# Kernel optimization log

Measured on AMD Instinct MI355X. Metric: run time of the kernel, lower is better.

Reference implementation:

```python
import jax, jax.numpy as jnp
import numpy as np

F = 1024
K = 32
N = 2048
EPS = 1e-6


def setup_inputs() -> dict:
    key = jax.random.key(0)
    ks = jax.random.split(key, 10)
    x = jax.random.normal(ks[0], (N, F), dtype=jnp.float32)
    idx = jax.random.randint(ks[1], (F, K), 0, F)
    norm_w = jnp.ones((F,), dtype=jnp.float32)
    w1 = jax.random.normal(ks[2], (F, K), dtype=jnp.float32) / np.sqrt(K)
    b1 = jnp.zeros((F,), dtype=jnp.float32)
    w2 = jax.random.normal(ks[3], (F, K), dtype=jnp.float32) / np.sqrt(K)
    b2 = jnp.zeros((F,), dtype=jnp.float32)
    amp = jnp.ones((F,), dtype=jnp.float32)
    freq = jnp.ones((F,), dtype=jnp.float32)
    decay = jnp.full((F,), 0.01, dtype=jnp.float32)
    alpha = jnp.ones((1,), dtype=jnp.float32)
    return {"x": x, "in_index_per_out": idx, "norm_w": norm_w,
            "w1": w1, "b1": b1, "amp": amp, "freq": freq, "decay": decay,
            "w2": w2, "b2": b2, "alpha": alpha}


def _rmsnorm(x, g):
    ms = jnp.mean(x * x, axis=-1, keepdims=True)
    return x * jax.lax.rsqrt(ms + EPS) * g


def _geo_sparse_linear(h, idx, w, b):
    hg = h[:, idx]
    return jnp.einsum('nok,ok->no', hg, w) + b


def _sine_param(z, amp, freq, decay):
    return amp * jnp.sin(freq * z) * jnp.exp(-decay * z * z)


def reference(x, in_index_per_out, norm_w, w1, b1, amp, freq, decay, w2, b2, alpha):
    h = _rmsnorm(x, norm_w)
    h = _sine_param(_geo_sparse_linear(h, in_index_per_out, w1, b1), amp, freq, decay)
    h = _geo_sparse_linear(h, in_index_per_out, w2, b2)
    return x + alpha * h
```

## Files before the change

### kernel.cpp

```cpp
#include <hip/hip_runtime.h>
#include <hip/hip_fp16.h>

#define FDIM 1024
#define KNZ 32
#define NROWS 2048
#define RB 8
#define TPB 1024
#define EPSV 1e-6f

static_assert(TPB == FDIM, "o = tid mapping requires TPB == FDIM");
static_assert(NROWS % RB == 0, "rows divide");

__device__ __forceinline__ unsigned int swz(unsigned int i) {
  return i ^ ((i >> 3) & 7u);
}

__device__ __forceinline__ unsigned f16bits(float f) {
  return (unsigned)__half_as_ushort(__float2half(f));
}

__global__ void geo_prep(const int* __restrict__ idx,
                         const float* __restrict__ w1,
                         const float* __restrict__ w2,
                         unsigned* __restrict__ pr1, unsigned* __restrict__ pr2) {
  const int tid = threadIdx.x;
  const int lane = tid & 63;
  const int grp = (lane >> 5);
  const int k = tid & 31;
  const int o = blockIdx.x * 8 + (tid >> 5);

  const unsigned off = swz((unsigned)idx[o * KNZ + k]);
  const int q = (int)(off & 7u);
  const int ob = o & 7;
  const int qr = (q - ob) & 7;

  const unsigned long long gmask = 0xFFFFFFFFull << (32 * grp);
  const unsigned long long lowmask = (1ull << lane) - 1ull;

  unsigned long long m[8];
  #pragma unroll
  for (int qq = 0; qq < 8; ++qq) m[qq] = __ballot(q == qq) & gmask;

  unsigned long long mym = 0;
  #pragma unroll
  for (int qq = 0; qq < 8; ++qq) mym = (q == qq) ? m[qq] : mym;
  const int r = __popcll(mym & lowmask);

  int pos = 0;
  #pragma unroll
  for (int qq = 0; qq < 8; ++qq) {
    const int c = (int)__popcll(m[qq]);
    const int qqr = (qq - ob) & 7;
    pos += (r < c) ? r : c;
    pos += (qqr < qr && c > r) ? 1 : 0;
  }

  const unsigned e1 = (f16bits(w1[o * KNZ + k]) << 16) | off;
  const unsigned e2 = (f16bits(w2[o * KNZ + k]) << 16) | off;
  pr1[pos * FDIM + o] = e1;
  pr2[pos * FDIM + o] = e2;
}

__device__ __forceinline__ void gatherh(unsigned e, const uint4* lds,
                                        __half2* acc2) {
  unsigned wd = (e & 0xFFFF0000u) | (e >> 16);
  __half2 w = *reinterpret_cast<__half2*>(&wd);
  uint4 hv = lds[e & 1023u];
  const unsigned* hd = reinterpret_cast<const unsigned*>(&hv);
  #pragma unroll
  for (int d = 0; d < 4; ++d) {
    __half2 h2 = *reinterpret_cast<const __half2*>(&hd[d]);
    acc2[d] = __hfma2(h2, w, acc2[d]);
  }
}

template <bool TR>
__global__ __launch_bounds__(TPB, 4)
void geo_main(const float* __restrict__ x, const float* __restrict__ norm_w,
              const float* __restrict__ b1, const float* __restrict__ amp,
              const float* __restrict__ freq, const float* __restrict__ decay,
              const float* __restrict__ b2, const float* __restrict__ alpha,
              const unsigned* __restrict__ pr1, const unsigned* __restrict__ pr2,
              const int* __restrict__ idx, const float* __restrict__ w1,
              const float* __restrict__ w2, float* __restrict__ out) {
  __shared__ uint4 h_lds[FDIM];
  __shared__ uint4 s_lds[FDIM];
  __shared__ float red[(TPB / 64) * RB];
  __shared__ float rs_sh[RB];

  const int tid = threadIdx.x;
  const int lane = tid & 63;
  const int wid = tid >> 6;
  const int r0 = blockIdx.x * RB;
  const int o = tid;

  {
    float v[RB];
    #pragma unroll
    for (int r = 0; r < RB; ++r)
      v[r] = x[(r0 + r) * FDIM + tid];

    const float g = norm_w[tid];

    float p[RB];
    #pragma unroll
    for (int r = 0; r < RB; ++r) p[r] = v[r] * v[r];
    #pragma unroll
    for (int r = 0; r < 4; ++r) {
      float up = __shfl_xor(p[r + 4], 4, 64);
      float dn = __shfl_xor(p[r], 4, 64);
      p[r] = (lane & 4) ? (p[r + 4] + up) : (p[r] + dn);
    }
    #pragma unroll
    for (int r = 0; r < 2; ++r) {
      float up = __shfl_xor(p[r + 2], 2, 64);
      float dn = __shfl_xor(p[r], 2, 64);
      p[r] = (lane & 2) ? (p[r + 2] + up) : (p[r] + dn);
    }
    {
      float up = __shfl_xor(p[1], 1, 64);
      float dn = __shfl_xor(p[0], 1, 64);
      p[0] = (lane & 1) ? (p[1] + up) : (p[0] + dn);
    }
    p[0] += __shfl_xor(p[0], 8, 64);
    p[0] += __shfl_xor(p[0], 16, 64);
    p[0] += __shfl_xor(p[0], 32, 64);
    if (lane < RB) red[wid * RB + lane] = p[0];

    uint4 h;
    __half2 h01 = __floats2half2_rn(g * v[0], g * v[1]);
    __half2 h23 = __floats2half2_rn(g * v[2], g * v[3]);
    __half2 h45 = __floats2half2_rn(g * v[4], g * v[5]);
    __half2 h67 = __floats2half2_rn(g * v[6], g * v[7]);
    h.x = *reinterpret_cast<unsigned*>(&h01);
    h.y = *reinterpret_cast<unsigned*>(&h23);
    h.z = *reinterpret_cast<unsigned*>(&h45);
    h.w = *reinterpret_cast<unsigned*>(&h67);
    h_lds[swz((unsigned)tid)] = h;
  }

  __syncthreads();

  {
    float a = red[lane] + red[64 + lane];
    a += __shfl_xor(a, 8, 64);
    a += __shfl_xor(a, 16, 64);
    a += __shfl_xor(a, 32, 64);
    if (lane < RB) rs_sh[lane] = rsqrtf(a * (1.0f / FDIM) + EPSV);
  }

  __half2 acc2[4];
  {
    unsigned z = 0;
    #pragma unroll
    for (int d = 0; d < 4; ++d) acc2[d] = *reinterpret_cast<__half2*>(&z);
  }

  if (TR) {
    #pragma unroll
    for (int gk = 0; gk < 4; ++gk) {
      unsigned u[8];
      #pragma unroll
      for (int j = 0; j < 8; ++j) u[j] = pr1[(gk * 8 + j) * FDIM + o];
      #pragma unroll
      for (int j = 0; j < 8; ++j) gatherh(u[j], h_lds, acc2);
    }
  } else {
    #pragma unroll 8
    for (int k = 0; k < KNZ; ++k) {
      unsigned off = swz((unsigned)idx[o * KNZ + k]);
      unsigned e = (f16bits(w1[o * KNZ + k]) << 16) | off;
      gatherh(e, h_lds, acc2);
    }
  }

  {
    const float bb1 = b1[o], am = amp[o], fq = freq[o], dc = decay[o];
    const float4 ra = *reinterpret_cast<const float4*>(&rs_sh[0]);
    const float4 rb = *reinterpret_cast<const float4*>(&rs_sh[4]);
    const float rsv[RB] = {ra.x, ra.y, ra.z, ra.w, rb.x, rb.y, rb.z, rb.w};
    float accf[RB];
    #pragma unroll
    for (int d = 0; d < 4; ++d) {
      float2 f = __half22float2(acc2[d]);
      accf[2 * d] = f.x; accf[2 * d + 1] = f.y;
    }
    float s[RB];
    #pragma unroll
    for (int r = 0; r < RB; ++r) {
      float z = fmaf(accf[r], rsv[r], bb1);
      s[r] = am * __sinf(fq * z) * __expf(-dc * z * z);
    }
    uint4 sv;
    __half2 s01 = __floats2half2_rn(s[0], s[1]);
    __half2 s23 = __floats2half2_rn(s[2], s[3]);
    __half2 s45 = __floats2half2_rn(s[4], s[5]);
    __half2 s67 = __floats2half2_rn(s[6], s[7]);
    sv.x = *reinterpret_cast<unsigned*>(&s01);
    sv.y = *reinterpret_cast<unsigned*>(&s23);
    sv.z = *reinterpret_cast<unsigned*>(&s45);
    sv.w = *reinterpret_cast<unsigned*>(&s67);
    s_lds[swz((unsigned)o)] = sv;
  }
  __syncthreads();

  {
    unsigned z = 0;
    #pragma unroll
    for (int d = 0; d < 4; ++d) acc2[d] = *reinterpret_cast<__half2*>(&z);
  }

  if (TR) {
    #pragma unroll
    for (int gk = 0; gk < 4; ++gk) {
      unsigned u[8];
      #pragma unroll
      for (int j = 0; j < 8; ++j) u[j] = pr2[(gk * 8 + j) * FDIM + o];
      #pragma unroll
      for (int j = 0; j < 8; ++j) gatherh(u[j], s_lds, acc2);
    }
  } else {
    #pragma unroll 8
    for (int k = 0; k < KNZ; ++k) {
      unsigned off = swz((unsigned)idx[o * KNZ + k]);
      unsigned e = (f16bits(w2[o * KNZ + k]) << 16) | off;
      gatherh(e, s_lds, acc2);
    }
  }

  {
    const float bb2 = b2[o];
    const float al = alpha[0];
    float accf[RB];
    #pragma unroll
    for (int d = 0; d < 4; ++d) {
      float2 f = __half22float2(acc2[d]);
      accf[2 * d] = f.x; accf[2 * d + 1] = f.y;
    }
    #pragma unroll
    for (int r = 0; r < RB; ++r)
      out[(r0 + r) * FDIM + o] =
          fmaf(al, accf[r] + bb2, x[(r0 + r) * FDIM + o]);
  }
}

extern "C" void kernel_launch(void* const* d_in, const int* in_sizes, int n_in,
                              void* d_out, int out_size, void* d_ws, size_t ws_size,
                              hipStream_t stream) {
  const float* x      = (const float*)d_in[0];
  const int*   idx    = (const int*)d_in[1];
  const float* norm_w = (const float*)d_in[2];
  const float* w1     = (const float*)d_in[3];
  const float* b1     = (const float*)d_in[4];
  const float* amp    = (const float*)d_in[5];
  const float* freq   = (const float*)d_in[6];
  const float* decay  = (const float*)d_in[7];
  const float* w2     = (const float*)d_in[8];
  const float* b2     = (const float*)d_in[9];
  const float* alpha  = (const float*)d_in[10];
  float* out = (float*)d_out;

  const size_t need = 2ull * FDIM * KNZ * sizeof(unsigned);
  if (ws_size >= need) {
    unsigned* pr1 = (unsigned*)d_ws;
    unsigned* pr2 = pr1 + (size_t)FDIM * KNZ;
    geo_prep<<<FDIM / 8, 256, 0, stream>>>(idx, w1, w2, pr1, pr2);
    geo_main<true><<<NROWS / RB, TPB, 0, stream>>>(
        x, norm_w, b1, amp, freq, decay, b2, alpha, pr1, pr2, idx, w1, w2, out);
  } else {
    geo_main<false><<<NROWS / RB, TPB, 0, stream>>>(
        x, norm_w, b1, amp, freq, decay, b2, alpha, nullptr, nullptr, idx, w1, w2, out);
  }
}
```

Before: 19.84 us.

## Halve rows per block to 4 and redo LDS bank-conflict sort for 8-byte entries

Rows per block drop from 8 to 4, so each LDS entry becomes a uint2 of four fp16 values instead of a uint4 of eight. The XOR swizzle is removed, and the prep kernel now sorts gather entries into 16 bank groups instead of 8 to spread conflicts for the smaller element size. The launch-bounds occupancy hint rises from 4 to 8 blocks and the grid doubles. The goal is more resident blocks and cheaper LDS traffic, at the cost of loading the index and weight stream twice as often per row.

```diff
diff --git a/kernel.cpp b/kernel.cpp
--- a/kernel.cpp
+++ b/kernel.cpp
@@ -4,19 +4,20 @@
 #define FDIM 1024
 #define KNZ 32
 #define NROWS 2048
-#define RB 8
+#define RB 4
 #define TPB 1024
 #define EPSV 1e-6f
 
 static_assert(TPB == FDIM, "o = tid mapping requires TPB == FDIM");
 static_assert(NROWS % RB == 0, "rows divide");
 
-__device__ __forceinline__ unsigned int swz(unsigned int i) {
-  return i ^ ((i >> 3) & 7u);
-}
-
 __device__ __forceinline__ unsigned f16bits(float f) {
   return (unsigned)__half_as_ushort(__float2half(f));
+}
+
+__device__ __forceinline__ unsigned packh2(float a, float b) {
+  __half2 h = __floats2half2_rn(a, b);
+  return *reinterpret_cast<unsigned*>(&h);
 }
 
 __global__ void geo_prep(const int* __restrict__ idx,
@@ -29,53 +30,49 @@
   const int k = tid & 31;
   const int o = blockIdx.x * 8 + (tid >> 5);
 
-  const unsigned off = swz((unsigned)idx[o * KNZ + k]);
-  const int q = (int)(off & 7u);
-  const int ob = o & 7;
-  const int qr = (q - ob) & 7;
+  const unsigned off = (unsigned)idx[o * KNZ + k] & 1023u;
+  const int q = (int)(off & 15u);
+  const int ob = o & 15;
+  const int qr = (q - ob) & 15;
 
   const unsigned long long gmask = 0xFFFFFFFFull << (32 * grp);
   const unsigned long long lowmask = (1ull << lane) - 1ull;
 
-  unsigned long long m[8];
+  unsigned long long m[16];
   #pragma unroll
-  for (int qq = 0; qq < 8; ++qq) m[qq] = __ballot(q == qq) & gmask;
+  for (int qq = 0; qq < 16; ++qq) m[qq] = __ballot(q == qq) & gmask;
 
   unsigned long long mym = 0;
   #pragma unroll
-  for (int qq = 0; qq < 8; ++qq) mym = (q == qq) ? m[qq] : mym;
+  for (int qq = 0; qq < 16; ++qq) mym = (q == qq) ? m[qq] : mym;
   const int r = __popcll(mym & lowmask);
 
   int pos = 0;
   #pragma unroll
-  for (int qq = 0; qq < 8; ++qq) {
+  for (int qq = 0; qq < 16; ++qq) {
     const int c = (int)__popcll(m[qq]);
-    const int qqr = (qq - ob) & 7;
+    const int qqr = (qq - ob) & 15;
     pos += (r < c) ? r : c;
     pos += (qqr < qr && c > r) ? 1 : 0;
   }
 
-  const unsigned e1 = (f16bits(w1[o * KNZ + k]) << 16) | off;
-  const unsigned e2 = (f16bits(w2[o * KNZ + k]) << 16) | off;
-  pr1[pos * FDIM + o] = e1;
-  pr2[pos * FDIM + o] = e2;
-}
-
-__device__ __forceinline__ void gatherh(unsigned e, const uint4* lds,
+  pr1[pos * FDIM + o] = (f16bits(w1[o * KNZ + k]) << 16) | off;
+  pr2[pos * FDIM + o] = (f16bits(w2[o * KNZ + k]) << 16) | off;
+}
+
+__device__ __forceinline__ void gatherh(unsigned e, const uint2* lds,
                                         __half2* acc2) {
   unsigned wd = (e & 0xFFFF0000u) | (e >> 16);
   __half2 w = *reinterpret_cast<__half2*>(&wd);
-  uint4 hv = lds[e & 1023u];
-  const unsigned* hd = reinterpret_cast<const unsigned*>(&hv);
-  #pragma unroll
-  for (int d = 0; d < 4; ++d) {
-    __half2 h2 = *reinterpret_cast<const __half2*>(&hd[d]);
-    acc2[d] = __hfma2(h2, w, acc2[d]);
-  }
+  uint2 hv = lds[e & 1023u];
+  __half2 h0 = *reinterpret_cast<const __half2*>(&hv.x);
+  __half2 h1 = *reinterpret_cast<const __half2*>(&hv.y);
+  acc2[0] = __hfma2(h0, w, acc2[0]);
+  acc2[1] = __hfma2(h1, w, acc2[1]);
 }
 
 template <bool TR>
-__global__ __launch_bounds__(TPB, 4)
+__global__ __launch_bounds__(TPB, 8)
 void geo_main(const float* __restrict__ x, const float* __restrict__ norm_w,
               const float* __restrict__ b1, const float* __restrict__ amp,
               const float* __restrict__ freq, const float* __restrict__ decay,
@@ -83,8 +80,8 @@
               const unsigned* __restrict__ pr1, const unsigned* __restrict__ pr2,
               const int* __restrict__ idx, const float* __restrict__ w1,
               const float* __restrict__ w2, float* __restrict__ out) {
-  __shared__ uint4 h_lds[FDIM];
-  __shared__ uint4 s_lds[FDIM];
+  __shared__ uint2 h_lds[FDIM];
+  __shared__ uint2 s_lds[FDIM];
   __shared__ float red[(TPB / 64) * RB];
   __shared__ float rs_sh[RB];
 
@@ -106,12 +103,6 @@
     #pragma unroll
     for (int r = 0; r < RB; ++r) p[r] = v[r] * v[r];
     #pragma unroll
-    for (int r = 0; r < 4; ++r) {
-      float up = __shfl_xor(p[r + 4], 4, 64);
-      float dn = __shfl_xor(p[r], 4, 64);
-      p[r] = (lane & 4) ? (p[r + 4] + up) : (p[r] + dn);
-    }
-    #pragma unroll
     for (int r = 0; r < 2; ++r) {
       float up = __shfl_xor(p[r + 2], 2, 64);
       float dn = __shfl_xor(p[r], 2, 64);
@@ -122,38 +113,34 @@
       float dn = __shfl_xor(p[0], 1, 64);
       p[0] = (lane & 1) ? (p[1] + up) : (p[0] + dn);
     }
+    p[0] += __shfl_xor(p[0], 4, 64);
     p[0] += __shfl_xor(p[0], 8, 64);
     p[0] += __shfl_xor(p[0], 16, 64);
     p[0] += __shfl_xor(p[0], 32, 64);
     if (lane < RB) red[wid * RB + lane] = p[0];
 
-    uint4 h;
-    __half2 h01 = __floats2half2_rn(g * v[0], g * v[1]);
-    __half2 h23 = __floats2half2_rn(g * v[2], g * v[3]);
-    __half2 h45 = __floats2half2_rn(g * v[4], g * v[5]);
-    __half2 h67 = __floats2half2_rn(g * v[6], g * v[7]);
-    h.x = *reinterpret_cast<unsigned*>(&h01);
-    h.y = *reinterpret_cast<unsigned*>(&h23);
-    h.z = *reinterpret_cast<unsigned*>(&h45);
-    h.w = *reinterpret_cast<unsigned*>(&h67);
-    h_lds[swz((unsigned)tid)] = h;
+    uint2 h;
+    h.x = packh2(g * v[0], g * v[1]);
+    h.y = packh2(g * v[2], g * v[3]);
+    h_lds[tid] = h;
   }
 
   __syncthreads();
 
   {
-    float a = red[lane] + red[64 + lane];
+    float a = red[lane];
+    a += __shfl_xor(a, 4, 64);
     a += __shfl_xor(a, 8, 64);
     a += __shfl_xor(a, 16, 64);
     a += __shfl_xor(a, 32, 64);
     if (lane < RB) rs_sh[lane] = rsqrtf(a * (1.0f / FDIM) + EPSV);
   }
 
-  __half2 acc2[4];
+  __half2 acc2[2];
   {
     unsigned z = 0;
-    #pragma unroll
-    for (int d = 0; d < 4; ++d) acc2[d] = *reinterpret_cast<__half2*>(&z);
+    acc2[0] = *reinterpret_cast<__half2*>(&z);
+    acc2[1] = *reinterpret_cast<__half2*>(&z);
   }
 
   if (TR) {
@@ -168,8 +155,8 @@
   } else {
     #pragma unroll 8
     for (int k = 0; k < KNZ; ++k) {
-      unsigned off = swz((unsigned)idx[o * KNZ + k]);
-      unsigned e = (f16bits(w1[o * KNZ + k]) << 16) | off;
+      unsigned e = (f16bits(w1[o * KNZ + k]) << 16) |
+                   ((unsigned)idx[o * KNZ + k] & 1023u);
       gatherh(e, h_lds, acc2);
     }
   }
@@ -177,13 +164,12 @@
   {
     const float bb1 = b1[o], am = amp[o], fq = freq[o], dc = decay[o];
     const float4 ra = *reinterpret_cast<const float4*>(&rs_sh[0]);
-    const float4 rb = *reinterpret_cast<const float4*>(&rs_sh[4]);
-    const float rsv[RB] = {ra.x, ra.y, ra.z, ra.w, rb.x, rb.y, rb.z, rb.w};
+    const float rsv[RB] = {ra.x, ra.y, ra.z, ra.w};
     float accf[RB];
-    #pragma unroll
-    for (int d = 0; d < 4; ++d) {
-      float2 f = __half22float2(acc2[d]);
-      accf[2 * d] = f.x; accf[2 * d + 1] = f.y;
+    {
+      float2 f0 = __half22float2(acc2[0]);
+      float2 f1 = __half22float2(acc2[1]);
+      accf[0] = f0.x; accf[1] = f0.y; accf[2] = f1.x; accf[3] = f1.y;
     }
     float s[RB];
     #pragma unroll
@@ -191,23 +177,17 @@
       float z = fmaf(accf[r], rsv[r], bb1);
       s[r] = am * __sinf(fq * z) * __expf(-dc * z * z);
     }
-    uint4 sv;
-    __half2 s01 = __floats2half2_rn(s[0], s[1]);
-    __half2 s23 = __floats2half2_rn(s[2], s[3]);
-    __half2 s45 = __floats2half2_rn(s[4], s[5]);
-    __half2 s67 = __floats2half2_rn(s[6], s[7]);
-    sv.x = *reinterpret_cast<unsigned*>(&s01);
-    sv.y = *reinterpret_cast<unsigned*>(&s23);
-    sv.z = *reinterpret_cast<unsigned*>(&s45);
-    sv.w = *reinterpret_cast<unsigned*>(&s67);
-    s_lds[swz((unsigned)o)] = sv;
+    uint2 sv;
+    sv.x = packh2(s[0], s[1]);
+    sv.y = packh2(s[2], s[3]);
+    s_lds[o] = sv;
   }
   __syncthreads();
 
   {
     unsigned z = 0;
-    #pragma unroll
-    for (int d = 0; d < 4; ++d) acc2[d] = *reinterpret_cast<__half2*>(&z);
+    acc2[0] = *reinterpret_cast<__half2*>(&z);
+    acc2[1] = *reinterpret_cast<__half2*>(&z);
   }
 
   if (TR) {
@@ -222,8 +202,8 @@
   } else {
     #pragma unroll 8
     for (int k = 0; k < KNZ; ++k) {
-      unsigned off = swz((unsigned)idx[o * KNZ + k]);
-      unsigned e = (f16bits(w2[o * KNZ + k]) << 16) | off;
+      unsigned e = (f16bits(w2[o * KNZ + k]) << 16) |
+                   ((unsigned)idx[o * KNZ + k] & 1023u);
       gatherh(e, s_lds, acc2);
     }
   }
@@ -232,10 +212,10 @@
     const float bb2 = b2[o];
     const float al = alpha[0];
     float accf[RB];
-    #pragma unroll
-    for (int d = 0; d < 4; ++d) {
-      float2 f = __half22float2(acc2[d]);
-      accf[2 * d] = f.x; accf[2 * d + 1] = f.y;
+    {
+      float2 f0 = __half22float2(acc2[0]);
+      float2 f1 = __half22float2(acc2[1]);
+      accf[0] = f0.x; accf[1] = f0.y; accf[2] = f1.x; accf[3] = f1.y;
     }
     #pragma unroll
     for (int r = 0; r < RB; ++r)
```

New measurement: 21.41 us. 1.08x slower.
